# Optimization experiments

Hardware: AMD Instinct MI355X
Metric: run time of the kernel (lower is better)

Reference implementation:

```python
import jax, jax.numpy as jnp
import numpy as np

N_NODES = 100000
N_EDGES = 1000000
D = 64            # node_hidden
IN_DIM = 4 * D    # 256
MLP_H = 32
EPS = 1e-5


def setup_inputs() -> dict:
    key = jax.random.key(0)
    ks = jax.random.split(key, 6)
    h = jax.random.normal(ks[0], (N_NODES, D), dtype=jnp.float32)
    edge_pairs = jax.random.randint(ks[1], (2, N_EDGES), 0, N_NODES, dtype=jnp.int64)
    # LayerNorm params
    gamma = jnp.ones((IN_DIM,), dtype=jnp.float32)
    beta = jnp.zeros((IN_DIM,), dtype=jnp.float32)
    # MLP params (PyTorch Linear default init: U(-1/sqrt(fan_in), 1/sqrt(fan_in)))
    b1_bound = 1.0 / np.sqrt(IN_DIM)
    W1 = jax.random.uniform(ks[2], (IN_DIM, MLP_H), minval=-b1_bound, maxval=b1_bound, dtype=jnp.float32)
    b1 = jax.random.uniform(ks[3], (MLP_H,), minval=-b1_bound, maxval=b1_bound, dtype=jnp.float32)
    b2_bound = 1.0 / np.sqrt(MLP_H)
    W2 = jax.random.uniform(ks[4], (MLP_H, 1), minval=-b2_bound, maxval=b2_bound, dtype=jnp.float32)
    b2 = jax.random.uniform(ks[5], (1,), minval=-b2_bound, maxval=b2_bound, dtype=jnp.float32)
    return {"h": h, "edge_pairs": edge_pairs, "gamma": gamma, "beta": beta,
            "W1": W1, "b1": b1, "W2": W2, "b2": b2}


def reference(h, edge_pairs, gamma, beta, W1, b1, W2, b2):
    u = h[edge_pairs[0]]                                    # [E, D]
    v = h[edge_pairs[1]]                                    # [E, D]
    feat = jnp.concatenate([u, v, jnp.abs(u - v), u * v], axis=-1)  # [E, 4D]
    mu = jnp.mean(feat, axis=-1, keepdims=True)
    var = jnp.mean(jnp.square(feat - mu), axis=-1, keepdims=True)
    feat = (feat - mu) * jax.lax.rsqrt(var + EPS) * gamma + beta
    hmid = jax.nn.relu(feat @ W1 + b1)                      # [E, MLP_H]; dropout inactive at eval
    logit = hmid @ W2 + b2                                  # [E, 1]
    return logit.reshape(-1)
```

## Files before the change

kernel.cpp:

```cpp
#include <hip/hip_runtime.h>
#include <hip/hip_bf16.h>

#define N_EDGES 1000000
#define N_TILES (N_EDGES / 16)
#define N_NODES 100000

typedef __attribute__((ext_vector_type(8))) short short8;
typedef __attribute__((ext_vector_type(4))) int intx4;
typedef __attribute__((ext_vector_type(4))) float floatx4;

__device__ __forceinline__ short f2bf(float f) {
    __bf16 b = (__bf16)f;
    return __builtin_bit_cast(short, b);
}

union BI { short8 s8; intx4 i4; __hip_bfloat162 b2[4]; };

__device__ __forceinline__ short8 dabs8(short8 a, short8 b) {
    BI ua, ub, ud;
    ua.s8 = a; ub.s8 = b;
#pragma unroll
    for (int i = 0; i < 4; ++i) ud.b2[i] = __hsub2(ua.b2[i], ub.b2[i]);
    ud.i4 &= 0x7fff7fff;
    return ud.s8;
}
__device__ __forceinline__ short8 pmul8(short8 a, short8 b) {
    BI ua, ub, up;
    ua.s8 = a; ub.s8 = b;
#pragma unroll
    for (int i = 0; i < 4; ++i) up.b2[i] = __hmul2(ua.b2[i], ub.b2[i]);
    return up.s8;
}

__global__ __launch_bounds__(256) void conv_kernel(const float* __restrict__ h,
                                                   unsigned short* __restrict__ hb) {
    const int i = blockIdx.x * blockDim.x + threadIdx.x;
    if (i >= (N_NODES * 64) / 8) return;
    const float* p = h + (long)i * 8;
    floatx4 a = *(const floatx4*)p;
    floatx4 b = *(const floatx4*)(p + 4);
    short8 o;
    o[0] = f2bf(a[0]); o[1] = f2bf(a[1]); o[2] = f2bf(a[2]); o[3] = f2bf(a[3]);
    o[4] = f2bf(b[0]); o[5] = f2bf(b[1]); o[6] = f2bf(b[2]); o[7] = f2bf(b[3]);
    *(short8*)(hb + (long)i * 8) = o;
}

__global__ __launch_bounds__(256) void wprep_kernel(const float* __restrict__ gamma,
                                                    const float* __restrict__ beta,
                                                    const float* __restrict__ W1,
                                                    unsigned short* __restrict__ Wt,
                                                    float* __restrict__ GB) {
    const int n = blockIdx.x;
    const int k = threadIdx.x;
    const float w1 = W1[k * 32 + n];
    float G = gamma[k] * w1;
    float B = beta[k] * w1;
    Wt[n * 256 + k] = (unsigned short)f2bf(G);
    G += __shfl_xor(G, 1);  B += __shfl_xor(B, 1);
    G += __shfl_xor(G, 2);  B += __shfl_xor(B, 2);
    G += __shfl_xor(G, 4);  B += __shfl_xor(B, 4);
    G += __shfl_xor(G, 8);  B += __shfl_xor(B, 8);
    G += __shfl_xor(G, 16); B += __shfl_xor(B, 16);
    G += __shfl_xor(G, 32); B += __shfl_xor(B, 32);
    __shared__ float sG[4], sB[4];
    if ((k & 63) == 0) { sG[k >> 6] = G; sB[k >> 6] = B; }
    __syncthreads();
    if (k == 0) {
        GB[n]      = sG[0] + sG[1] + sG[2] + sG[3];
        GB[32 + n] = sB[0] + sB[1] + sB[2] + sB[3];
    }
}

__global__ __launch_bounds__(256) void edgehead_kernel(
    const unsigned short* __restrict__ hb,
    const int* __restrict__ ep,
    const float* __restrict__ b1,
    const float* __restrict__ W2,
    const float* __restrict__ b2p,
    const unsigned short* __restrict__ Wt,
    const float* __restrict__ GB,
    float* __restrict__ out)
{
    const int lane = threadIdx.x & 63;
    const int c = lane & 15;
    const int q = lane >> 4;
    const int wid = (int)((blockIdx.x * blockDim.x + threadIdx.x) >> 6);
    const int nw = (int)((gridDim.x * blockDim.x) >> 6);

    __shared__ short lds_wt[32 * 33 * 8];
    for (int idx = threadIdx.x; idx < 1024; idx += 256) {
        const int r = idx >> 5, j = idx & 31;
        *(short8*)(lds_wt + (r * 33 + j) * 8) = *(const short8*)(Wt + r * 256 + 8 * j);
    }
    __syncthreads();

    int wt_off = (c * 33 + q) * 8;
    short8 ones;
#pragma unroll
    for (int j = 0; j < 8; ++j) ones[j] = (short)0x3F80;

    short8 wsel;
#pragma unroll
    for (int j = 0; j < 8; ++j) wsel[j] = (c == 4 * q + (j & 3)) ? (short)0x3F80 : (short)0;

    const float Gn0 = GB[c],      Gn1 = GB[16 + c];
    const float Bn0 = GB[32 + c] + b1[c];
    const float Bn1 = GB[48 + c] + b1[16 + c];
    const float W20 = W2[c],      W21 = W2[16 + c];
    const float b2  = b2p[0];

    int t = wid;
    if (t >= N_TILES) return;

#define IDX_LOAD(tt, S, D) { int _t = (tt); if (_t >= N_TILES) _t = wid;          \
                             const int _e = _t * 16 + c;                          \
                             S = ep[_e]; D = ep[N_EDGES + _e]; }
#define ROW_ISSUE(S, D, U0, U1, V0, V1)                                           \
    U0 = *(const short8*)(hb + (long)(S) * 64 + 8 * q);                           \
    U1 = *(const short8*)(hb + (long)(S) * 64 + 8 * q + 32);                      \
    V0 = *(const short8*)(hb + (long)(D) * 64 + 8 * q);                           \
    V1 = *(const short8*)(hb + (long)(D) * 64 + 8 * q + 32);

    short8 aU0, aU1, aV0, aV1;
    short8 bU0, bU1, bV0, bV1;
    short8 cU0, cU1, cV0, cV1;
    int sA, dA, sB, dB, sC, dC;

    IDX_LOAD(t,          sA, dA);
    IDX_LOAD(t + nw,     sB, dB);
    IDX_LOAD(t + 2 * nw, sC, dC);
    ROW_ISSUE(sA, dA, aU0, aU1, aV0, aV1);
    ROW_ISSUE(sB, dB, bU0, bU1, bV0, bV1);
    IDX_LOAD(t + 3 * nw, sA, dA);
    IDX_LOAD(t + 4 * nw, sB, dB);

#define BODY(U0, U1, V0, V1, NU0, NU1, NV0, NV1, SN, DN)                          \
  {                                                                               \
    if (t >= N_TILES) goto tail;                                                  \
    asm("" : "+v"(wt_off));        \
    ROW_ISSUE(SN, DN, NU0, NU1, NV0, NV1);                                        \
    IDX_LOAD(t + 5 * nw, SN, DN);                                                 \
    floatx4 acc0 = {0.f, 0.f, 0.f, 0.f};                                          \
    floatx4 acc1 = {0.f, 0.f, 0.f, 0.f};                                          \
    floatx4 asum = {0.f, 0.f, 0.f, 0.f};                            \
    floatx4 agrm = {0.f, 0.f, 0.f, 0.f};         \
    _Pragma("unroll")                                                             \
    for (int s = 0; s < 8; ++s) {                                                 \
      short8 af;                                                                  \
      switch (s) {                                                                \
        case 0: af = U0; break;                                                   \
        case 1: af = U1; break;                                                   \
        case 2: af = V0; break;                                                   \
        case 3: af = V1; break;                                                   \
        case 4: af = dabs8(U0, V0); break;           \
        case 5: af = dabs8(U1, V1); break;                                        \
        case 6: af = pmul8(U0, V0); break;                                        \
        default: af = pmul8(U1, V1); break;                                       \
      }                                                                           \
      const short8 bf0 = *(const short8*)(lds_wt + wt_off + s * 32);              \
      const short8 bf1 = *(const short8*)(lds_wt + wt_off + 16 * 33 * 8 + s * 32);\
      acc0 = __builtin_amdgcn_mfma_f32_16x16x32_bf16(af, bf0,  acc0, 0, 0, 0);    \
      acc1 = __builtin_amdgcn_mfma_f32_16x16x32_bf16(af, bf1,  acc1, 0, 0, 0);    \
      asum = __builtin_amdgcn_mfma_f32_16x16x32_bf16(af, ones, asum, 0, 0, 0);    \
      agrm = __builtin_amdgcn_mfma_f32_16x16x32_bf16(af, af,   agrm, 0, 0, 0);    \
    }                                                                             \
    float ss[4];                                                                  \
    _Pragma("unroll")                                                             \
    for (int r = 0; r < 4; ++r) ss[r] = __shfl(agrm[r], 20 * q + r);              \
    short8 af2;                                                                   \
    _Pragma("unroll")                                                             \
    for (int r = 0; r < 4; ++r) {                                                 \
      const float mu  = asum[r] * (1.f / 256.f);                                  \
      const float var = fmaf(ss[r], 1.f / 256.f, -mu * mu);                       \
      const float rs  = rsqrtf(var + 1e-5f);                                      \
      float h0 = fmaf(rs, fmaf(-mu, Gn0, acc0[r]), Bn0); h0 = fmaxf(h0, 0.f);     \
      float h1 = fmaf(rs, fmaf(-mu, Gn1, acc1[r]), Bn1); h1 = fmaxf(h1, 0.f);     \
      af2[r]     = f2bf(h0 * W20);                                                \
      af2[4 + r] = f2bf(h1 * W21);                                                \
    }                                                                             \
    floatx4 dfin = {0.f, 0.f, 0.f, 0.f};                                          \
    dfin = __builtin_amdgcn_mfma_f32_16x16x32_bf16(af2, wsel, dfin, 0, 0, 0);     \
    float part = (dfin[0] + dfin[1]) + (dfin[2] + dfin[3]);                       \
    part += __shfl_xor(part, 16);                                                 \
    part += __shfl_xor(part, 32);                                                 \
    if (q == 0) out[t * 16 + c] = part + b2;             \
    t += nw;                                                                      \
  }

    for (;;) {
        BODY(aU0, aU1, aV0, aV1, cU0, cU1, cV0, cV1, sC, dC);
        BODY(bU0, bU1, bV0, bV1, aU0, aU1, aV0, aV1, sA, dA);
        BODY(cU0, cU1, cV0, cV1, bU0, bU1, bV0, bV1, sB, dB);
    }
tail:
    return;
#undef BODY
#undef ROW_ISSUE
#undef IDX_LOAD
}

extern "C" void kernel_launch(void* const* d_in, const int* in_sizes, int n_in,
                              void* d_out, int out_size, void* d_ws, size_t ws_size,
                              hipStream_t stream) {
    const float* h     = (const float*)d_in[0];
    const int*   ep    = (const int*)d_in[1];
    const float* gamma = (const float*)d_in[2];
    const float* beta  = (const float*)d_in[3];
    const float* W1    = (const float*)d_in[4];
    const float* b1    = (const float*)d_in[5];
    const float* W2    = (const float*)d_in[6];
    const float* b2    = (const float*)d_in[7];
    float* out = (float*)d_out;

    unsigned short* hb = (unsigned short*)d_ws;
    unsigned short* Wt = (unsigned short*)((char*)d_ws + 12800000);
    float* GB = (float*)((char*)d_ws + 12800000 + 16384);

    conv_kernel<<<(N_NODES * 64 / 8 + 255) / 256, 256, 0, stream>>>(h, hb);
    wprep_kernel<<<32, 256, 0, stream>>>(gamma, beta, W1, Wt, GB);
    edgehead_kernel<<<2048, 256, 0, stream>>>(hb, ep, b1, W2, b2, Wt, GB, out);
}
```

Baseline: 134.0 us.

## Merge prep kernels into one launch and shorten gather prefetch to double-buffer

The bf16 conversion kernel and the weight-prep kernel become a single launch that dispatches on block index, which removes one kernel launch and its inter-kernel gap. The edge kernel's software pipeline goes from triple-buffered row gathers to double-buffered, with the index prefetch distance cut from five to three tiles. This lowers register pressure and may allow higher occupancy, but leaves less latency hiding for the random gathers.

```diff
diff --git a/kernel.cpp b/kernel.cpp
--- a/kernel.cpp
+++ b/kernel.cpp
@@ -4,6 +4,7 @@
 #define N_EDGES 1000000
 #define N_TILES (N_EDGES / 16)
 #define N_NODES 100000
+#define CONV_BLOCKS ((N_NODES * 64 / 8) / 256)
 
 typedef __attribute__((ext_vector_type(8))) short short8;
 typedef __attribute__((ext_vector_type(4))) int intx4;
@@ -32,25 +33,24 @@
     return up.s8;
 }
 
-__global__ __launch_bounds__(256) void conv_kernel(const float* __restrict__ h,
-                                                   unsigned short* __restrict__ hb) {
-    const int i = blockIdx.x * blockDim.x + threadIdx.x;
-    if (i >= (N_NODES * 64) / 8) return;
-    const float* p = h + (long)i * 8;
-    floatx4 a = *(const floatx4*)p;
-    floatx4 b = *(const floatx4*)(p + 4);
-    short8 o;
-    o[0] = f2bf(a[0]); o[1] = f2bf(a[1]); o[2] = f2bf(a[2]); o[3] = f2bf(a[3]);
-    o[4] = f2bf(b[0]); o[5] = f2bf(b[1]); o[6] = f2bf(b[2]); o[7] = f2bf(b[3]);
-    *(short8*)(hb + (long)i * 8) = o;
-}
-
-__global__ __launch_bounds__(256) void wprep_kernel(const float* __restrict__ gamma,
-                                                    const float* __restrict__ beta,
-                                                    const float* __restrict__ W1,
-                                                    unsigned short* __restrict__ Wt,
-                                                    float* __restrict__ GB) {
-    const int n = blockIdx.x;
+__global__ __launch_bounds__(256) void prep_kernel(
+    const float* __restrict__ h, unsigned short* __restrict__ hb,
+    const float* __restrict__ gamma, const float* __restrict__ beta,
+    const float* __restrict__ W1, unsigned short* __restrict__ Wt,
+    float* __restrict__ GB)
+{
+    if (blockIdx.x < CONV_BLOCKS) {
+        const int i = blockIdx.x * blockDim.x + threadIdx.x;
+        const float* p = h + (long)i * 8;
+        floatx4 a = *(const floatx4*)p;
+        floatx4 b = *(const floatx4*)(p + 4);
+        short8 o;
+        o[0] = f2bf(a[0]); o[1] = f2bf(a[1]); o[2] = f2bf(a[2]); o[3] = f2bf(a[3]);
+        o[4] = f2bf(b[0]); o[5] = f2bf(b[1]); o[6] = f2bf(b[2]); o[7] = f2bf(b[3]);
+        *(short8*)(hb + (long)i * 8) = o;
+        return;
+    }
+    const int n = blockIdx.x - CONV_BLOCKS;
     const int k = threadIdx.x;
     const float w1 = W1[k * 32 + n];
     float G = gamma[k] * w1;
@@ -123,23 +123,19 @@
 
     short8 aU0, aU1, aV0, aV1;
     short8 bU0, bU1, bV0, bV1;
-    short8 cU0, cU1, cV0, cV1;
-    int sA, dA, sB, dB, sC, dC;
-
-    IDX_LOAD(t,          sA, dA);
+    int sA, dA, sB, dB;
+
+    IDX_LOAD(t, sA, dA);
+    ROW_ISSUE(sA, dA, aU0, aU1, aV0, aV1);
     IDX_LOAD(t + nw,     sB, dB);
-    IDX_LOAD(t + 2 * nw, sC, dC);
-    ROW_ISSUE(sA, dA, aU0, aU1, aV0, aV1);
-    ROW_ISSUE(sB, dB, bU0, bU1, bV0, bV1);
-    IDX_LOAD(t + 3 * nw, sA, dA);
-    IDX_LOAD(t + 4 * nw, sB, dB);
+    IDX_LOAD(t + 2 * nw, sA, dA);
 
 #define BODY(U0, U1, V0, V1, NU0, NU1, NV0, NV1, SN, DN)                          \
   {                                                                               \
     if (t >= N_TILES) goto tail;                                                  \
     asm("" : "+v"(wt_off));        \
     ROW_ISSUE(SN, DN, NU0, NU1, NV0, NV1);                                        \
-    IDX_LOAD(t + 5 * nw, SN, DN);                                                 \
+    IDX_LOAD(t + 3 * nw, SN, DN);                                                 \
     floatx4 acc0 = {0.f, 0.f, 0.f, 0.f};                                          \
     floatx4 acc1 = {0.f, 0.f, 0.f, 0.f};                                          \
     floatx4 asum = {0.f, 0.f, 0.f, 0.f};                            \
@@ -188,9 +184,8 @@
   }
 
     for (;;) {
-        BODY(aU0, aU1, aV0, aV1, cU0, cU1, cV0, cV1, sC, dC);
+        BODY(aU0, aU1, aV0, aV1, bU0, bU1, bV0, bV1, sB, dB);
         BODY(bU0, bU1, bV0, bV1, aU0, aU1, aV0, aV1, sA, dA);
-        BODY(cU0, cU1, cV0, cV1, bU0, bU1, bV0, bV1, sB, dB);
     }
 tail:
     return;
@@ -216,7 +211,6 @@
     unsigned short* Wt = (unsigned short*)((char*)d_ws + 12800000);
     float* GB = (float*)((char*)d_ws + 12800000 + 16384);
 
-    conv_kernel<<<(N_NODES * 64 / 8 + 255) / 256, 256, 0, stream>>>(h, hb);
-    wprep_kernel<<<32, 256, 0, stream>>>(gamma, beta, W1, Wt, GB);
+    prep_kernel<<<CONV_BLOCKS + 32, 256, 0, stream>>>(h, hb, gamma, beta, W1, Wt, GB);
     edgehead_kernel<<<2048, 256, 0, stream>>>(hb, ep, b1, W2, b2, Wt, GB, out);
 }
```

New measurement: 132.0 us. No clear change (-1.5%).
